# Optimization experiments

Measured on AMD Instinct MI355X. Metric: run time of the kernel, lower is better.

## Reference

```python
import jax, jax.numpy as jnp
import numpy as np

ALPHA = 0.5  # config_param['alpha']


def setup_inputs() -> dict:
    key = jax.random.key(0)
    ks = jax.random.split(key, 10)
    B, T, N, E, H = 64, 20, 8192, 128, 128
    # sparse multi-hot basket indicators
    x = (jax.random.uniform(ks[0], (B, T, N)) < 0.01).astype(jnp.float32)
    seq_len = jax.random.randint(ks[1], (B,), 1, T + 1)  # pack_padded requires >=1
    A = jax.random.uniform(ks[2], (N, N), dtype=jnp.float32) * 0.01  # dense item-item adjacency
    W1 = jax.random.normal(ks[3], (E, N), dtype=jnp.float32) * 0.02
    b1 = jnp.zeros((E,), jnp.float32)
    W2 = jax.random.normal(ks[4], (E, N), dtype=jnp.float32) * 0.02
    b2 = jnp.zeros((E,), jnp.float32)
    W_ih = jax.random.normal(ks[5], (4 * H, E), dtype=jnp.float32) * 0.05
    W_hh = jax.random.normal(ks[6], (4 * H, H), dtype=jnp.float32) * 0.05
    b_ih = jnp.zeros((4 * H,), jnp.float32)
    b_hh = jnp.zeros((4 * H,), jnp.float32)
    W_out = jax.random.normal(ks[7], (N, H), dtype=jnp.float32) * 0.02
    I_B = jnp.ones((N,), jnp.float32) / N  # item_probs-style bias init
    threshold = jnp.array([0.005], jnp.float32)  # adj_matrix.mean()
    return dict(x=x, seq_len=seq_len, A=A, W1=W1, b1=b1, W2=W2, b2=b2,
                W_ih=W_ih, W_hh=W_hh, b_ih=b_ih, b_hh=b_hh,
                W_out=W_out, I_B=I_B, threshold=threshold)


def reference(x, seq_len, A, W1, b1, W2, b2, W_ih, W_hh, b_ih, b_hh, W_out, I_B, threshold):
    B, T, N = x.shape
    H = W_hh.shape[1]
    xf = x.reshape(B * T, N)
    # two basket encoders, elementwise max combine (dropout = identity in eval)
    e1 = jax.nn.relu(xf @ W1.T + b1)
    e2 = jax.nn.relu(xf @ W2.T + b2)
    basket = jnp.maximum(e1, e2).reshape(B, T, -1)  # [B, T, E]

    # 1-layer LSTM (torch gate order i,f,g,o); packed variable-length seqs
    # emulated by freezing (h, c) once t >= seq_len, so h_n matches pack_padded.
    valid = jnp.arange(T)[:, None] < seq_len[None, :]  # [T, B]
    xs = basket.transpose(1, 0, 2)                     # [T, B, E]
    b = b_ih + b_hh

    def step(carry, inp):
        h, c = carry
        x_t, v = inp
        gates = x_t @ W_ih.T + h @ W_hh.T + b
        i, f, g, o = jnp.split(gates, 4, axis=-1)
        c_new = jax.nn.sigmoid(f) * c + jax.nn.sigmoid(i) * jnp.tanh(g)
        h_new = jax.nn.sigmoid(o) * jnp.tanh(c_new)
        m = v[:, None]
        return (jnp.where(m, h_new, h), jnp.where(m, c_new, c)), None

    h0 = jnp.zeros((B, H), x.dtype)
    c0 = jnp.zeros((B, H), x.dtype)
    (h_n, _), _ = jax.lax.scan(step, (h0, c0), (xs, valid))

    p = jax.nn.sigmoid(h_n @ W_out.T)  # [B, N]
    # mm(p, diag(relu(I_B))) is algebraically an elementwise scale
    predict = (1.0 - ALPHA) * p + ALPHA * (p * jax.nn.relu(I_B) + jax.nn.relu(p @ A))
    return predict
```

## Files before the change

kernel.cpp:

```cpp
#include <hip/hip_runtime.h>
#include <hip/hip_bf16.h>
#include <stdint.h>

#define B_ 64
#define T_ 20
#define N_ 8192
#define E_ 128
#define H_ 128
#define G4 512
#define SPLITK 8

typedef short bf16x8 __attribute__((ext_vector_type(8)));
typedef float f32x4 __attribute__((ext_vector_type(4)));

__device__ __forceinline__ float sigmoidf_(float x){ return 1.0f/(1.0f+expf(-x)); }

__device__ __forceinline__ unsigned short f2bf(float f){
  union { float f; uint32_t u; } v; v.f = f;
  uint32_t u = v.u;
  uint32_t r = (u + 0x7FFFu + ((u >> 16) & 1u)) >> 16;
  return (unsigned short)r;
}
__device__ __forceinline__ uint32_t pk2(float a, float b){
  return (uint32_t)f2bf(a) | ((uint32_t)f2bf(b) << 16);
}
__device__ __forceinline__ float bf2f(unsigned short s){
  union { uint32_t u; float f; } v; v.u = ((uint32_t)s) << 16; return v.f;
}

__global__ void k_transpose(const float* __restrict__ W1, const float* __restrict__ W2,
                            unsigned short* __restrict__ W12T){
  __shared__ float t1[128][33];
  __shared__ float t2[128][33];
  int n0 = blockIdx.x * 32;
  int tid = threadIdx.x;
  int nl = tid & 31, eg = tid >> 5;
  for (int i = 0; i < 16; i++){
    int e = eg * 16 + i;
    t1[e][nl] = W1[(size_t)e*N_ + n0 + nl];
    t2[e][nl] = W2[(size_t)e*N_ + n0 + nl];
  }
  __syncthreads();
  for (int n = 0; n < 32; n++){
    float v = (tid < 128) ? t1[tid][n] : t2[tid-128][n];
    W12T[(size_t)(n0+n)*256 + tid] = f2bf(v);
  }
}

__global__ void k_mlp(const float* __restrict__ x, const int* __restrict__ seq_len,
                      const unsigned short* __restrict__ W12T, const float* __restrict__ b1,
                      const float* __restrict__ b2, float* __restrict__ basket){
  int bt = blockIdx.x;
  int b = bt / T_, t = bt % T_;
  int tid = threadIdx.x;
  if (t >= seq_len[b]){
    if (tid < 128) basket[(size_t)bt*E_ + tid] = 0.f;
    return;
  }
  __shared__ int idxs[1024];
  __shared__ int cnt;
  __shared__ float e2s[128];
  if (tid == 0) cnt = 0;
  __syncthreads();
  const float4* xr = (const float4*)(x + (size_t)bt * N_);
  for (int i = 0; i < 8; i++){
    float4 v = xr[i*256 + tid];
    int base = (i*256 + tid)*4;
    if (v.x != 0.f){ int q = atomicAdd(&cnt,1); idxs[q] = base;   }
    if (v.y != 0.f){ int q = atomicAdd(&cnt,1); idxs[q] = base+1; }
    if (v.z != 0.f){ int q = atomicAdd(&cnt,1); idxs[q] = base+2; }
    if (v.w != 0.f){ int q = atomicAdd(&cnt,1); idxs[q] = base+3; }
  }
  __syncthreads();
  int m = cnt; if (m > 1024) m = 1024;
  float acc = (tid < 128) ? b1[tid] : b2[tid-128];
  int i = 0;
  for (; i + 8 <= m; i += 8){
    int j0 = idxs[i+0], j1 = idxs[i+1], j2 = idxs[i+2], j3 = idxs[i+3];
    int j4 = idxs[i+4], j5 = idxs[i+5], j6 = idxs[i+6], j7 = idxs[i+7];
    float v0 = bf2f(W12T[(size_t)j0*256 + tid]);
    float v1 = bf2f(W12T[(size_t)j1*256 + tid]);
    float v2 = bf2f(W12T[(size_t)j2*256 + tid]);
    float v3 = bf2f(W12T[(size_t)j3*256 + tid]);
    float v4 = bf2f(W12T[(size_t)j4*256 + tid]);
    float v5 = bf2f(W12T[(size_t)j5*256 + tid]);
    float v6 = bf2f(W12T[(size_t)j6*256 + tid]);
    float v7 = bf2f(W12T[(size_t)j7*256 + tid]);
    acc += ((v0+v1)+(v2+v3)) + ((v4+v5)+(v6+v7));
  }
  for (; i < m; i++)
    acc += bf2f(W12T[(size_t)idxs[i]*256 + tid]);
  acc = fmaxf(acc, 0.f);
  if (tid >= 128) e2s[tid-128] = acc;
  __syncthreads();
  if (tid < 128) basket[(size_t)bt*E_ + tid] = fmaxf(acc, e2s[tid]);
}

__global__ void __launch_bounds__(512, 1)
k_lstmx(const int* __restrict__ seq_len, const float* __restrict__ basket,
        const float* __restrict__ W_ih, const float* __restrict__ b_ih,
        const float* __restrict__ b_hh, const float* __restrict__ W_hh,
        float* __restrict__ hn){
  int b = blockIdx.x;
  int L = seq_len[b];
  int j = threadIdx.x;
  __shared__ float bsk[T_][E_];
  __shared__ float XpL[T_][G4];
  __shared__ float hs[128];
  __shared__ float gs[512];
  for (int idx = j; idx < T_*E_; idx += 512)
    bsk[idx>>7][idx&127] = basket[((size_t)b*T_ + (idx>>7))*E_ + (idx&127)];
  __syncthreads();
  {
    float bias = b_ih[j] + b_hh[j];
    float accv[T_];
    #pragma unroll
    for (int tt = 0; tt < T_; tt++) accv[tt] = bias;
    const float4* wr = (const float4*)(W_ih + (size_t)j * E_);
    for (int k4 = 0; k4 < 32; k4++){
      float4 w = wr[k4];
      #pragma unroll
      for (int tt = 0; tt < T_; tt++){
        float4 h = *(const float4*)&bsk[tt][k4*4];
        accv[tt] += w.x*h.x + w.y*h.y + w.z*h.z + w.w*h.w;
      }
    }
    #pragma unroll
    for (int tt = 0; tt < T_; tt++) XpL[tt][j] = accv[tt];
  }
  float4 whh[32];
  const float4* wr2 = (const float4*)(W_hh + (size_t)j * H_);
  #pragma unroll
  for (int k = 0; k < 32; k++) whh[k] = wr2[k];
  if (j < 128) hs[j] = 0.f;
  float c = 0.f;
  __syncthreads();
  for (int t = 0; t < L; t++){
    float s0 = XpL[t][j], s1 = 0.f, s2 = 0.f, s3 = 0.f;
    #pragma unroll
    for (int k = 0; k < 32; k += 4){
      float4 w, h;
      w = whh[k+0]; h = *(const float4*)&hs[k*4+ 0]; s0 += w.x*h.x + w.y*h.y + w.z*h.z + w.w*h.w;
      w = whh[k+1]; h = *(const float4*)&hs[k*4+ 4]; s1 += w.x*h.x + w.y*h.y + w.z*h.z + w.w*h.w;
      w = whh[k+2]; h = *(const float4*)&hs[k*4+ 8]; s2 += w.x*h.x + w.y*h.y + w.z*h.z + w.w*h.w;
      w = whh[k+3]; h = *(const float4*)&hs[k*4+12]; s3 += w.x*h.x + w.y*h.y + w.z*h.z + w.w*h.w;
    }
    gs[j] = (s0 + s1) + (s2 + s3);
    __syncthreads();
    if (j < 128){
      float i_ = gs[j], f_ = gs[128+j], gg = gs[256+j], o_ = gs[384+j];
      c = sigmoidf_(f_)*c + sigmoidf_(i_)*tanhf(gg);
      hs[j] = sigmoidf_(o_)*tanhf(c);
    }
    __syncthreads();
  }
  if (j < 128) hn[(size_t)b*H_ + j] = hs[j];
}

__global__ void k_pout(const float* __restrict__ hn, const float* __restrict__ W_out,
                       unsigned short* __restrict__ pbf){
  __shared__ unsigned short hb[64*128];
  int tid = threadIdx.x;
  {
    int row = tid >> 2;
    int k16 = (tid & 3) * 32;
    const float4* hr = (const float4*)(hn + (size_t)row*H_ + k16);
    #pragma unroll
    for (int i = 0; i < 4; i++){
      float4 a = hr[i*2], bq = hr[i*2+1];
      uint4 u; u.x = pk2(a.x,a.y); u.y = pk2(a.z,a.w); u.z = pk2(bq.x,bq.y); u.w = pk2(bq.z,bq.w);
      int blk = (k16 >> 3) + i;
      *(uint4*)&hb[row*128 + ((blk ^ (row & 7)) * 8)] = u;
    }
  }
  __syncthreads();
  int w = tid >> 6, l = tid & 63;
  int n0 = blockIdx.x * 128;
  f32x4 acc[8];
  #pragma unroll
  for (int i = 0; i < 8; i++) acc[i] = (f32x4){0.f,0.f,0.f,0.f};
  int row = w*16 + (l & 15);
  #pragma unroll
  for (int ks = 0; ks < 4; ks++){
    int kk = ks*32 + (l >> 4)*8;
    int blk = kk >> 3;
    bf16x8 af = *(bf16x8*)&hb[row*128 + ((blk ^ (row & 7)) * 8)];
    #pragma unroll
    for (int nt = 0; nt < 8; nt++){
      int n = n0 + nt*16 + (l & 15);
      const float4* wp = (const float4*)(W_out + (size_t)n*H_ + kk);
      float4 wa = wp[0], wb = wp[1];
      union { uint4 u; bf16x8 v; } cc;
      cc.u.x = pk2(wa.x,wa.y); cc.u.y = pk2(wa.z,wa.w);
      cc.u.z = pk2(wb.x,wb.y); cc.u.w = pk2(wb.z,wb.w);
      acc[nt] = __builtin_amdgcn_mfma_f32_16x16x32_bf16(af, cc.v, acc[nt], 0, 0, 0);
    }
  }
  #pragma unroll
  for (int nt = 0; nt < 8; nt++){
    int n = n0 + nt*16 + (l & 15);
    #pragma unroll
    for (int r = 0; r < 4; r++){
      int rr = w*16 + (l >> 4)*4 + r;
      float pv = 1.f/(1.f + expf(-acc[nt][r]));
      pbf[(size_t)rr*N_ + n] = f2bf(pv);
    }
  }
}

#define ISSUE(a0,a1,a2,a3,pr,kb) do {                                          \
    pr = *(const uint4*)&pbf[(size_t)prow*N_ + (kb) + c8*8];                   \
    const float* bse = Ag + (size_t)(kb)*N_ + (size_t)kq*16*N_ + n0 + sn;      \
    a0.x = bse[0];              a0.y = bse[(size_t)N_];                        \
    a0.z = bse[(size_t)2*N_];   a0.w = bse[(size_t)3*N_];                      \
    a1.x = bse[(size_t)4*N_];   a1.y = bse[(size_t)5*N_];                      \
    a1.z = bse[(size_t)6*N_];   a1.w = bse[(size_t)7*N_];                      \
    a2.x = bse[(size_t)8*N_];   a2.y = bse[(size_t)9*N_];                      \
    a2.z = bse[(size_t)10*N_];  a2.w = bse[(size_t)11*N_];                     \
    a3.x = bse[(size_t)12*N_];  a3.y = bse[(size_t)13*N_];                     \
    a3.z = bse[(size_t)14*N_];  a3.w = bse[(size_t)15*N_];                     \
  } while(0)

#define STAGE(abf,ptb,a0,a1,a2,a3,pr) do {                                     \
    *(uint4*)&ptb[prow*64 + ((c8*8) ^ ((prow & 7)*8))] = pr;                   \
    uint2 u0, u1, u2, u3;                                                      \
    u0.x = pk2(a0.x,a0.y); u0.y = pk2(a0.z,a0.w);                              \
    u1.x = pk2(a1.x,a1.y); u1.y = pk2(a1.z,a1.w);                              \
    u2.x = pk2(a2.x,a2.y); u2.y = pk2(a2.z,a2.w);                              \
    u3.x = pk2(a3.x,a3.y); u3.y = pk2(a3.z,a3.w);                              \
    int kb0 = kq*16;                                                           \
    *(uint2*)&abf[sn*64 + ((kb0+ 0) ^ ((sn & 7)*8))] = u0;                     \
    *(uint2*)&abf[sn*64 + ((kb0+ 4) ^ ((sn & 7)*8))] = u1;                     \
    *(uint2*)&abf[sn*64 + ((kb0+ 8) ^ ((sn & 7)*8))] = u2;                     \
    *(uint2*)&abf[sn*64 + ((kb0+12) ^ ((sn & 7)*8))] = u3;                     \
  } while(0)

#define SYNC_AND() do {                                                        \
    asm volatile("s_waitcnt lgkmcnt(0)" ::: "memory");                         \
    __builtin_amdgcn_sched_barrier(0);                                         \
    __builtin_amdgcn_s_barrier();                                              \
    __builtin_amdgcn_sched_barrier(0);                                         \
  } while(0)

__global__ void __launch_bounds__(512, 4)
k_gemm(const unsigned short* __restrict__ pbf, const float* __restrict__ Ag,
       float* __restrict__ Cp){
  __shared__ unsigned short Abf0[128*64];
  __shared__ unsigned short Abf1[128*64];
  __shared__ unsigned short pt0[64*64];
  __shared__ unsigned short pt1[64*64];
  int tid = threadIdx.x;
  int nb = blockIdx.x & 63, ks = blockIdx.x >> 6;
  int n0 = nb * 128;
  int kbase = ks * (N_ / SPLITK);
  int sn = tid & 127, kq = tid >> 7;
  int prow = tid >> 3, c8 = tid & 7;
  int w = tid >> 6, l = tid & 63;
  int wm = w >> 2, wn = w & 3;
  f32x4 acc00 = {0,0,0,0}, acc01 = {0,0,0,0}, acc10 = {0,0,0,0}, acc11 = {0,0,0,0};
  float* Cout = Cp + (size_t)ks * (B_ * N_);
  const int NSTEP = (N_ / SPLITK) / 64;

  f32x4 aA0, aA1, aA2, aA3, aB0, aB1, aB2, aB3;
  uint4 pA, pB;

  auto compute = [&](const unsigned short* abf, const unsigned short* ptb){
    #pragma unroll
    for (int kc = 0; kc < 64; kc += 32){
      int ko = kc + (l >> 4)*8;
      bf16x8 af0, af1, bf0, bf1;
      {
        int r0 = wm*32 + (l & 15);
        int r1 = r0 + 16;
        af0 = *(const bf16x8*)&ptb[r0*64 + (ko ^ ((r0 & 7)*8))];
        af1 = *(const bf16x8*)&ptb[r1*64 + (ko ^ ((r1 & 7)*8))];
        int n0_ = wn*32 + (l & 15);
        int n1_ = n0_ + 16;
        bf0 = *(const bf16x8*)&abf[n0_*64 + (ko ^ ((n0_ & 7)*8))];
        bf1 = *(const bf16x8*)&abf[n1_*64 + (ko ^ ((n1_ & 7)*8))];
      }
      acc00 = __builtin_amdgcn_mfma_f32_16x16x32_bf16(af0, bf0, acc00, 0, 0, 0);
      acc01 = __builtin_amdgcn_mfma_f32_16x16x32_bf16(af0, bf1, acc01, 0, 0, 0);
      acc10 = __builtin_amdgcn_mfma_f32_16x16x32_bf16(af1, bf0, acc10, 0, 0, 0);
      acc11 = __builtin_amdgcn_mfma_f32_16x16x32_bf16(af1, bf1, acc11, 0, 0, 0);
    }
  };

  ISSUE(aA0,aA1,aA2,aA3,pA, kbase);
  for (int s = 0; s < NSTEP; s += 2){
    if (s + 1 < NSTEP) ISSUE(aB0,aB1,aB2,aB3,pB, kbase + (s+1)*64);
    STAGE(Abf0, pt0, aA0,aA1,aA2,aA3, pA);
    SYNC_AND();
    compute(Abf0, pt0);
    if (s + 2 < NSTEP) ISSUE(aA0,aA1,aA2,aA3,pA, kbase + (s+2)*64);
    STAGE(Abf1, pt1, aB0,aB1,aB2,aB3, pB);
    SYNC_AND();
    compute(Abf1, pt1);
  }

  {
    int n_a = n0 + wn*32 + (l & 15);
    int n_b = n_a + 16;
    int rbase = wm*32 + (l >> 4)*4;
    #pragma unroll
    for (int r = 0; r < 4; r++){
      Cout[(size_t)(rbase + r)*N_ + n_a]      = acc00[r];
      Cout[(size_t)(rbase + r)*N_ + n_b]      = acc01[r];
      Cout[(size_t)(rbase + 16 + r)*N_ + n_a] = acc10[r];
      Cout[(size_t)(rbase + 16 + r)*N_ + n_b] = acc11[r];
    }
  }
}

__global__ void k_final(const unsigned short* __restrict__ pbf, const float* __restrict__ Cp,
                        const float* __restrict__ I_B, float* __restrict__ out){
  int idx = blockIdx.x*256 + threadIdx.x;
  ushort4 pu = ((const ushort4*)pbf)[idx];
  float4 cv = {0.f, 0.f, 0.f, 0.f};
  #pragma unroll
  for (int s = 0; s < SPLITK; s++){
    float4 v = ((const float4*)(Cp + (size_t)s * (B_ * N_)))[idx];
    cv.x += v.x; cv.y += v.y; cv.z += v.z; cv.w += v.w;
  }
  int n = (idx*4) & (N_-1);
  float4 ib = *(const float4*)&I_B[n];
  float4 o;
  float p0 = bf2f(pu.x), p1 = bf2f(pu.y), p2 = bf2f(pu.z), p3 = bf2f(pu.w);
  o.x = 0.5f*p0 + 0.5f*(p0*fmaxf(ib.x,0.f) + fmaxf(cv.x,0.f));
  o.y = 0.5f*p1 + 0.5f*(p1*fmaxf(ib.y,0.f) + fmaxf(cv.y,0.f));
  o.z = 0.5f*p2 + 0.5f*(p2*fmaxf(ib.z,0.f) + fmaxf(cv.z,0.f));
  o.w = 0.5f*p3 + 0.5f*(p3*fmaxf(ib.w,0.f) + fmaxf(cv.w,0.f));
  ((float4*)out)[idx] = o;
}

extern "C" void kernel_launch(void* const* d_in, const int* in_sizes, int n_in,
                              void* d_out, int out_size, void* d_ws, size_t ws_size,
                              hipStream_t stream) {
  const float* x     = (const float*)d_in[0];
  const int*   seq   = (const int*)  d_in[1];
  const float* A     = (const float*)d_in[2];
  const float* W1    = (const float*)d_in[3];
  const float* b1    = (const float*)d_in[4];
  const float* W2    = (const float*)d_in[5];
  const float* b2    = (const float*)d_in[6];
  const float* W_ih  = (const float*)d_in[7];
  const float* W_hh  = (const float*)d_in[8];
  const float* b_ih  = (const float*)d_in[9];
  const float* b_hh  = (const float*)d_in[10];
  const float* W_out = (const float*)d_in[11];
  const float* I_B   = (const float*)d_in[12];
  float* out = (float*)d_out;

  float* ws = (float*)d_ws;
  unsigned short* W12T = (unsigned short*)ws;
  float* basket = ws + 1048576;
  float* hn     = basket + 163840;
  float* Cp     = hn + 8192;
  unsigned short* pbf = (unsigned short*)(Cp + 4194304);

  k_transpose<<<256, 256, 0, stream>>>(W1, W2, W12T);
  k_mlp      <<<1280,256, 0, stream>>>(x, seq, W12T, b1, b2, basket);
  k_lstmx    <<<64,  512, 0, stream>>>(seq, basket, W_ih, b_ih, b_hh, W_hh, hn);
  k_pout     <<<64,  256, 0, stream>>>(hn, W_out, pbf);
  k_gemm     <<<64*SPLITK, 512, 0, stream>>>(pbf, A, Cp);
  k_final    <<<512, 256, 0, stream>>>(pbf, Cp, I_B, out);
}
```

Baseline: 149.8 us.

## Drop split-K in p@A GEMM and fuse final epilogue into GEMM

The split-K GEMM (512 blocks of 128 columns, with 8 K-partials written to a workspace) and the separate reduction/epilogue kernel are replaced by one kernel. Each of 256 blocks now owns 32 output columns over the full K=8192 and applies the relu/I_B/alpha epilogue directly. This removes the 16 MB partial-sum write and read-back and one launch. In exchange each block runs a 64-step serial K loop with only one MFMA accumulator per wave, so per-block latency and lower occupancy may limit streaming of A.

```diff
diff --git a/kernel.cpp b/kernel.cpp
--- a/kernel.cpp
+++ b/kernel.cpp
@@ -8,7 +8,6 @@
 #define E_ 128
 #define H_ 128
 #define G4 512
-#define SPLITK 8
 
 typedef short bf16x8 __attribute__((ext_vector_type(8)));
 typedef float f32x4 __attribute__((ext_vector_type(4)));
@@ -208,31 +207,22 @@
   }
 }
 
-#define ISSUE(a0,a1,a2,a3,pr,kb) do {                                          \
-    pr = *(const uint4*)&pbf[(size_t)prow*N_ + (kb) + c8*8];                   \
-    const float* bse = Ag + (size_t)(kb)*N_ + (size_t)kq*16*N_ + n0 + sn;      \
-    a0.x = bse[0];              a0.y = bse[(size_t)N_];                        \
-    a0.z = bse[(size_t)2*N_];   a0.w = bse[(size_t)3*N_];                      \
-    a1.x = bse[(size_t)4*N_];   a1.y = bse[(size_t)5*N_];                      \
-    a1.z = bse[(size_t)6*N_];   a1.w = bse[(size_t)7*N_];                      \
-    a2.x = bse[(size_t)8*N_];   a2.y = bse[(size_t)9*N_];                      \
-    a2.z = bse[(size_t)10*N_];  a2.w = bse[(size_t)11*N_];                     \
-    a3.x = bse[(size_t)12*N_];  a3.y = bse[(size_t)13*N_];                     \
-    a3.z = bse[(size_t)14*N_];  a3.w = bse[(size_t)15*N_];                     \
+#define ISSUEF(q0,q1,r0,r1,kb) do {                                            \
+    r0 = *(const uint4*)&pbf[(size_t)prow*N_ + (kb) + c8*8];                   \
+    r1 = *(const uint4*)&pbf[(size_t)prow*N_ + (kb) + 64 + c8*8];              \
+    const float* bse = Ag + (size_t)((kb) + kq*8)*N_ + n0 + sn;                \
+    q0.x = bse[0];               q0.y = bse[(size_t)N_];                       \
+    q0.z = bse[2*(size_t)N_];    q0.w = bse[3*(size_t)N_];                     \
+    q1.x = bse[4*(size_t)N_];    q1.y = bse[5*(size_t)N_];                     \
+    q1.z = bse[6*(size_t)N_];    q1.w = bse[7*(size_t)N_];                     \
   } while(0)
 
-#define STAGE(abf,ptb,a0,a1,a2,a3,pr) do {                                     \
-    *(uint4*)&ptb[prow*64 + ((c8*8) ^ ((prow & 7)*8))] = pr;                   \
-    uint2 u0, u1, u2, u3;                                                      \
-    u0.x = pk2(a0.x,a0.y); u0.y = pk2(a0.z,a0.w);                              \
-    u1.x = pk2(a1.x,a1.y); u1.y = pk2(a1.z,a1.w);                              \
-    u2.x = pk2(a2.x,a2.y); u2.y = pk2(a2.z,a2.w);                              \
-    u3.x = pk2(a3.x,a3.y); u3.y = pk2(a3.z,a3.w);                              \
-    int kb0 = kq*16;                                                           \
-    *(uint2*)&abf[sn*64 + ((kb0+ 0) ^ ((sn & 7)*8))] = u0;                     \
-    *(uint2*)&abf[sn*64 + ((kb0+ 4) ^ ((sn & 7)*8))] = u1;                     \
-    *(uint2*)&abf[sn*64 + ((kb0+ 8) ^ ((sn & 7)*8))] = u2;                     \
-    *(uint2*)&abf[sn*64 + ((kb0+12) ^ ((sn & 7)*8))] = u3;                     \
+#define STAGEF(abf,ptb,q0,q1,r0,r1) do {                                       \
+    *(uint4*)&ptb[prow*128 + ((c8*8) ^ swp)]        = r0;                      \
+    *(uint4*)&ptb[prow*128 + ((64 + c8*8) ^ swp)]   = r1;                      \
+    uint4 v; v.x = pk2(q0.x,q0.y); v.y = pk2(q0.z,q0.w);                       \
+    v.z = pk2(q1.x,q1.y); v.w = pk2(q1.z,q1.w);                                \
+    *(uint4*)&abf[sn*128 + ((kq*8) ^ swa)] = v;                                \
   } while(0)
 
 #define SYNC_AND() do {                                                        \
@@ -243,94 +233,65 @@
   } while(0)
 
 __global__ void __launch_bounds__(512, 4)
-k_gemm(const unsigned short* __restrict__ pbf, const float* __restrict__ Ag,
-       float* __restrict__ Cp){
-  __shared__ unsigned short Abf0[128*64];
-  __shared__ unsigned short Abf1[128*64];
-  __shared__ unsigned short pt0[64*64];
-  __shared__ unsigned short pt1[64*64];
+k_gemmf(const unsigned short* __restrict__ pbf, const float* __restrict__ Ag,
+        const float* __restrict__ I_B, float* __restrict__ out){
+  __shared__ unsigned short abf0[32*128];
+  __shared__ unsigned short abf1[32*128];
+  __shared__ unsigned short pt0[64*128];
+  __shared__ unsigned short pt1[64*128];
   int tid = threadIdx.x;
-  int nb = blockIdx.x & 63, ks = blockIdx.x >> 6;
-  int n0 = nb * 128;
-  int kbase = ks * (N_ / SPLITK);
-  int sn = tid & 127, kq = tid >> 7;
+  int nb = blockIdx.x;
+  int n0 = nb * 32;
+  int sn = tid & 31, kq = tid >> 5;
   int prow = tid >> 3, c8 = tid & 7;
+  int swp = (prow & 7) * 8;
+  int swa = (sn & 7) * 8;
   int w = tid >> 6, l = tid & 63;
-  int wm = w >> 2, wn = w & 3;
-  f32x4 acc00 = {0,0,0,0}, acc01 = {0,0,0,0}, acc10 = {0,0,0,0}, acc11 = {0,0,0,0};
-  float* Cout = Cp + (size_t)ks * (B_ * N_);
-  const int NSTEP = (N_ / SPLITK) / 64;
-
-  f32x4 aA0, aA1, aA2, aA3, aB0, aB1, aB2, aB3;
-  uint4 pA, pB;
+  int wm = w >> 1, wn = w & 1;
+  f32x4 acc = {0.f, 0.f, 0.f, 0.f};
+  const int NSTEP = N_ / 128;
+
+  f32x4 aA0, aA1, aB0, aB1;
+  uint4 pA0, pA1, pB0, pB1;
+
+  int m_  = wm*16 + (l & 15);
+  int nn_ = wn*16 + (l & 15);
+  int swm = (m_ & 7) * 8;
+  int swn = (nn_ & 7) * 8;
 
   auto compute = [&](const unsigned short* abf, const unsigned short* ptb){
     #pragma unroll
-    for (int kc = 0; kc < 64; kc += 32){
+    for (int kc = 0; kc < 128; kc += 32){
       int ko = kc + (l >> 4)*8;
-      bf16x8 af0, af1, bf0, bf1;
-      {
-        int r0 = wm*32 + (l & 15);
-        int r1 = r0 + 16;
-        af0 = *(const bf16x8*)&ptb[r0*64 + (ko ^ ((r0 & 7)*8))];
-        af1 = *(const bf16x8*)&ptb[r1*64 + (ko ^ ((r1 & 7)*8))];
-        int n0_ = wn*32 + (l & 15);
-        int n1_ = n0_ + 16;
-        bf0 = *(const bf16x8*)&abf[n0_*64 + (ko ^ ((n0_ & 7)*8))];
-        bf1 = *(const bf16x8*)&abf[n1_*64 + (ko ^ ((n1_ & 7)*8))];
-      }
-      acc00 = __builtin_amdgcn_mfma_f32_16x16x32_bf16(af0, bf0, acc00, 0, 0, 0);
-      acc01 = __builtin_amdgcn_mfma_f32_16x16x32_bf16(af0, bf1, acc01, 0, 0, 0);
-      acc10 = __builtin_amdgcn_mfma_f32_16x16x32_bf16(af1, bf0, acc10, 0, 0, 0);
-      acc11 = __builtin_amdgcn_mfma_f32_16x16x32_bf16(af1, bf1, acc11, 0, 0, 0);
+      bf16x8 af = *(const bf16x8*)&ptb[m_*128 + (ko ^ swm)];
+      bf16x8 bf = *(const bf16x8*)&abf[nn_*128 + (ko ^ swn)];
+      acc = __builtin_amdgcn_mfma_f32_16x16x32_bf16(af, bf, acc, 0, 0, 0);
     }
   };
 
-  ISSUE(aA0,aA1,aA2,aA3,pA, kbase);
+  ISSUEF(aA0,aA1,pA0,pA1, 0);
   for (int s = 0; s < NSTEP; s += 2){
-    if (s + 1 < NSTEP) ISSUE(aB0,aB1,aB2,aB3,pB, kbase + (s+1)*64);
-    STAGE(Abf0, pt0, aA0,aA1,aA2,aA3, pA);
+    if (s + 1 < NSTEP) ISSUEF(aB0,aB1,pB0,pB1, (s+1)*128);
+    STAGEF(abf0, pt0, aA0,aA1, pA0,pA1);
     SYNC_AND();
-    compute(Abf0, pt0);
-    if (s + 2 < NSTEP) ISSUE(aA0,aA1,aA2,aA3,pA, kbase + (s+2)*64);
-    STAGE(Abf1, pt1, aB0,aB1,aB2,aB3, pB);
+    compute(abf0, pt0);
+    if (s + 2 < NSTEP) ISSUEF(aA0,aA1,pA0,pA1, (s+2)*128);
+    STAGEF(abf1, pt1, aB0,aB1, pB0,pB1);
     SYNC_AND();
-    compute(Abf1, pt1);
+    compute(abf1, pt1);
   }
 
   {
-    int n_a = n0 + wn*32 + (l & 15);
-    int n_b = n_a + 16;
-    int rbase = wm*32 + (l >> 4)*4;
-    #pragma unroll
-    for (int r = 0; r < 4; r++){
-      Cout[(size_t)(rbase + r)*N_ + n_a]      = acc00[r];
-      Cout[(size_t)(rbase + r)*N_ + n_b]      = acc01[r];
-      Cout[(size_t)(rbase + 16 + r)*N_ + n_a] = acc10[r];
-      Cout[(size_t)(rbase + 16 + r)*N_ + n_b] = acc11[r];
-    }
-  }
-}
-
-__global__ void k_final(const unsigned short* __restrict__ pbf, const float* __restrict__ Cp,
-                        const float* __restrict__ I_B, float* __restrict__ out){
-  int idx = blockIdx.x*256 + threadIdx.x;
-  ushort4 pu = ((const ushort4*)pbf)[idx];
-  float4 cv = {0.f, 0.f, 0.f, 0.f};
-  #pragma unroll
-  for (int s = 0; s < SPLITK; s++){
-    float4 v = ((const float4*)(Cp + (size_t)s * (B_ * N_)))[idx];
-    cv.x += v.x; cv.y += v.y; cv.z += v.z; cv.w += v.w;
-  }
-  int n = (idx*4) & (N_-1);
-  float4 ib = *(const float4*)&I_B[n];
-  float4 o;
-  float p0 = bf2f(pu.x), p1 = bf2f(pu.y), p2 = bf2f(pu.z), p3 = bf2f(pu.w);
-  o.x = 0.5f*p0 + 0.5f*(p0*fmaxf(ib.x,0.f) + fmaxf(cv.x,0.f));
-  o.y = 0.5f*p1 + 0.5f*(p1*fmaxf(ib.y,0.f) + fmaxf(cv.y,0.f));
-  o.z = 0.5f*p2 + 0.5f*(p2*fmaxf(ib.z,0.f) + fmaxf(cv.z,0.f));
-  o.w = 0.5f*p3 + 0.5f*(p3*fmaxf(ib.w,0.f) + fmaxf(cv.w,0.f));
-  ((float4*)out)[idx] = o;
+    int col = n0 + wn*16 + (l & 15);
+    float ib = fmaxf(I_B[col], 0.f);
+    #pragma unroll
+    for (int q = 0; q < 4; q++){
+      int row = wm*16 + (l >> 4)*4 + q;
+      float pv = bf2f(pbf[(size_t)row*N_ + col]);
+      float cv = fmaxf(acc[q], 0.f);
+      out[(size_t)row*N_ + col] = 0.5f*pv + 0.5f*(pv*ib + cv);
+    }
+  }
 }
 
 extern "C" void kernel_launch(void* const* d_in, const int* in_sizes, int n_in,
@@ -355,13 +316,11 @@
   unsigned short* W12T = (unsigned short*)ws;
   float* basket = ws + 1048576;
   float* hn     = basket + 163840;
-  float* Cp     = hn + 8192;
-  unsigned short* pbf = (unsigned short*)(Cp + 4194304);
+  unsigned short* pbf = (unsigned short*)(hn + 8192);
 
   k_transpose<<<256, 256, 0, stream>>>(W1, W2, W12T);
   k_mlp      <<<1280,256, 0, stream>>>(x, seq, W12T, b1, b2, basket);
   k_lstmx    <<<64,  512, 0, stream>>>(seq, basket, W_ih, b_ih, b_hh, W_hh, hn);
   k_pout     <<<64,  256, 0, stream>>>(hn, W_out, pbf);
-  k_gemm     <<<64*SPLITK, 512, 0, stream>>>(pbf, A, Cp);
-  k_final    <<<512, 256, 0, stream>>>(pbf, Cp, I_B, out);
-}
+  k_gemmf    <<<256, 512, 0, stream>>>(pbf, A, I_B, out);
+}
```

After: 163.6 us. 1.09x slower.
